# Kernel tuning notes

Hardware: AMD Instinct MI355X
Metric: run time of the kernel (lower is better)

Reference implementation:

```python
import jax, jax.numpy as jnp
import numpy as np

N_NODES = 50000
IN_CH, HID_CH, OUT_CH = 128, 128, 16
N_EDGES = 800000


def setup_inputs() -> dict:
    key = jax.random.key(0)
    ks = jax.random.split(key, 10)
    def lin_w(k, fan_in, fan_out):
        bound = 1.0 / np.sqrt(fan_in)
        return jax.random.uniform(k, (fan_in, fan_out), jnp.float32, -bound, bound)
    inp = {
        'x': jax.random.normal(ks[0], (N_NODES, IN_CH), jnp.float32),
        'edge_index': jax.random.randint(ks[1], (2, N_EDGES), 0, N_NODES, jnp.int64),
        # SAGEConv l/r weights: lin_l (neighbor aggregate, with bias), lin_r (root, no bias)
        'W1_l': lin_w(ks[2], IN_CH, HID_CH), 'b1': jnp.zeros((HID_CH,), jnp.float32),
        'W1_r': lin_w(ks[3], IN_CH, HID_CH),
        'W2_l': lin_w(ks[4], HID_CH, HID_CH), 'b2': jnp.zeros((HID_CH,), jnp.float32),
        'W2_r': lin_w(ks[5], HID_CH, HID_CH),
        'W3_l': lin_w(ks[6], HID_CH, HID_CH), 'b3': jnp.zeros((HID_CH,), jnp.float32),
        'W3_r': lin_w(ks[7], HID_CH, HID_CH),
        'W_lin': lin_w(ks[8], HID_CH, OUT_CH), 'b_lin': jnp.zeros((OUT_CH,), jnp.float32),
    }
    return inp


def _sage_conv(x, src, dst, W_l, b_l, W_r, n_nodes):
    # mean aggregation of source-node features at destination nodes
    msg_sum = jax.ops.segment_sum(x[src], dst, num_segments=n_nodes)  # [N, d]
    deg = jax.ops.segment_sum(jnp.ones((src.shape[0],), x.dtype), dst, num_segments=n_nodes)
    mean = msg_sum / jnp.maximum(deg, 1.0)[:, None]
    return mean @ W_l + b_l + x @ W_r


def reference(x, edge_index, W1_l, b1, W1_r, W2_l, b2, W2_r, W3_l, b3, W3_r, W_lin, b_lin):
    src, dst = edge_index[0], edge_index[1]
    n = x.shape[0]
    h = jax.nn.relu(_sage_conv(x, src, dst, W1_l, b1, W1_r, n))
    h = jax.nn.relu(_sage_conv(h, src, dst, W2_l, b2, W2_r, n))
    # dropout is identity in eval mode
    h = jax.nn.relu(_sage_conv(h, src, dst, W3_l, b3, W3_r, n))
    return h @ W_lin + b_lin
```

## Files before the change

### kernel.cpp

```cpp
#include <hip/hip_runtime.h>


typedef short bf16x8 __attribute__((ext_vector_type(8)));
typedef float f32x4 __attribute__((ext_vector_type(4)));

__device__ __forceinline__ float bf16_to_f32(unsigned int lo16) {
  unsigned int u = lo16 << 16;
  return __builtin_bit_cast(float, u);
}
__device__ __forceinline__ unsigned short f32_to_bf16(float f) {
  unsigned int u = __builtin_bit_cast(unsigned int, f);
  unsigned int r = (u + 0x7FFFu + ((u >> 16) & 1u)) >> 16;
  return (unsigned short)r;
}

__device__ __forceinline__ void gload_lds16(const void* g, void* lds_base) {
  __builtin_amdgcn_global_load_lds(
      (__attribute__((address_space(1))) unsigned int*)(uintptr_t)g,
      (__attribute__((address_space(3))) unsigned int*)(unsigned int)(uintptr_t)lds_base,
      16, 0, 0);
}

__global__ void k_zero_i32(int* __restrict__ p, int n) {
  int i = blockIdx.x * blockDim.x + threadIdx.x;
  if (i < n) p[i] = 0;
}

__global__ __launch_bounds__(256) void k_split(const float* __restrict__ in,
                                               unsigned short* __restrict__ hi,
                                               unsigned short* __restrict__ lo, int n4) {
  int i = blockIdx.x * blockDim.x + threadIdx.x;
  if (i < n4) {
    float4 v = *reinterpret_cast<const float4*>(&in[(size_t)i * 4]);
    ushort4 h, l;
    h.x = f32_to_bf16(v.x); l.x = f32_to_bf16(v.x - bf16_to_f32(h.x));
    h.y = f32_to_bf16(v.y); l.y = f32_to_bf16(v.y - bf16_to_f32(h.y));
    h.z = f32_to_bf16(v.z); l.z = f32_to_bf16(v.z - bf16_to_f32(h.z));
    h.w = f32_to_bf16(v.w); l.w = f32_to_bf16(v.w - bf16_to_f32(h.w));
    *reinterpret_cast<ushort4*>(&hi[(size_t)i * 4]) = h;
    *reinterpret_cast<ushort4*>(&lo[(size_t)i * 4]) = l;
  }
}

__global__ __launch_bounds__(256) void k_prep_w3(
    const float* __restrict__ W1l, const float* __restrict__ W1r,
    const float* __restrict__ W2l, const float* __restrict__ W2r,
    const float* __restrict__ W3l, const float* __restrict__ W3r,
    unsigned short* __restrict__ Whi1, unsigned short* __restrict__ Wlo1,
    unsigned short* __restrict__ Whi2, unsigned short* __restrict__ Wlo2,
    unsigned short* __restrict__ Whi3, unsigned short* __restrict__ Wlo3) {
  int layer = blockIdx.x >> 7;
  int n = blockIdx.x & 127;
  int k = threadIdx.x;
  const float* Wl = (layer == 0) ? W1l : (layer == 1) ? W2l : W3l;
  const float* Wr = (layer == 0) ? W1r : (layer == 1) ? W2r : W3r;
  unsigned short* Whi = (layer == 0) ? Whi1 : (layer == 1) ? Whi2 : Whi3;
  unsigned short* Wlo = (layer == 0) ? Wlo1 : (layer == 1) ? Wlo2 : Wlo3;
  float v = (k < 128) ? Wl[(size_t)k * 128 + n] : Wr[(size_t)(k - 128) * 128 + n];
  unsigned short h = f32_to_bf16(v);
  Whi[(size_t)n * 256 + k] = h;
  Wlo[(size_t)n * 256 + k] = f32_to_bf16(v - bf16_to_f32(h));
}

__global__ void k_detect(const int* __restrict__ ei, int* __restrict__ flag) {
  int t = threadIdx.x;
  if (t == 0) *flag = 0;
  __syncthreads();
  int any = 0;
  for (int i = t; i < 1024; i += 256)
    if (ei[2 * i + 1] != 0) any = 1;
  if (any) atomicOr(flag, 1);
}

__device__ __forceinline__ int load_src(const int* ei, int E, int i, int is32) {
  return is32 ? ei[i] : ei[2 * i];
}
__device__ __forceinline__ int load_dst(const int* ei, int E, int i, int is32) {
  return is32 ? ei[E + i] : ei[2 * E + 2 * i];
}

__global__ __launch_bounds__(256) void k_count(const int* __restrict__ ei,
                                               const int* __restrict__ flag,
                                               int* __restrict__ deg,
                                               int* __restrict__ erank, int E) {
  int i = blockIdx.x * blockDim.x + threadIdx.x;
  if (i < E) {
    int is32 = *flag;
    erank[i] = atomicAdd(&deg[load_dst(ei, E, i, is32)], 1);
  }
}

__global__ __launch_bounds__(256) void k_scan1(const int* __restrict__ deg,
                                               int* __restrict__ bsum, int N) {
  __shared__ int s[256];
  int t = threadIdx.x;
  int base = blockIdx.x * 1024 + t * 4;
  int v = 0;
#pragma unroll
  for (int j = 0; j < 4; ++j) {
    int i = base + j;
    v += (i < N) ? deg[i] : 0;
  }
  s[t] = v;
  __syncthreads();
  for (int off = 128; off > 0; off >>= 1) {
    if (t < off) s[t] += s[t + off];
    __syncthreads();
  }
  if (t == 0) bsum[blockIdx.x] = s[0];
}

__global__ __launch_bounds__(1024) void k_scan2(int* __restrict__ bsum,
                                                int* __restrict__ row_ptr,
                                                int nb, int N) {
  __shared__ int s[1024];
  int t = threadIdx.x;
  int v = (t < nb) ? bsum[t] : 0;
  s[t] = v;
  __syncthreads();
  for (int off = 1; off < 1024; off <<= 1) {
    int add = (t >= off) ? s[t - off] : 0;
    __syncthreads();
    s[t] += add;
    __syncthreads();
  }
  if (t < nb) bsum[t] = s[t] - v;
  if (t == 1023) row_ptr[N] = s[1023];
}

__global__ __launch_bounds__(256) void k_scan3(const int* __restrict__ deg,
                                               const int* __restrict__ bsum,
                                               int* __restrict__ row_ptr,
                                               float* __restrict__ inv_deg, int N) {
  __shared__ int s[256];
  int t = threadIdx.x;
  int base = blockIdx.x * 1024 + t * 4;
  int v[4];
  int sum = 0;
#pragma unroll
  for (int j = 0; j < 4; ++j) {
    int i = base + j;
    v[j] = (i < N) ? deg[i] : 0;
    sum += v[j];
  }
  s[t] = sum;
  __syncthreads();
  for (int off = 1; off < 256; off <<= 1) {
    int add = (t >= off) ? s[t - off] : 0;
    __syncthreads();
    s[t] += add;
    __syncthreads();
  }
  int excl = s[t] - sum + bsum[blockIdx.x];
#pragma unroll
  for (int j = 0; j < 4; ++j) {
    int i = base + j;
    if (i < N) {
      row_ptr[i] = excl;
      inv_deg[i] = 1.0f / (float)((v[j] > 1) ? v[j] : 1);
      excl += v[j];
    }
  }
}

__global__ __launch_bounds__(256) void k_fill(const int* __restrict__ ei,
                                              const int* __restrict__ flag,
                                              const int* __restrict__ row_ptr,
                                              const int* __restrict__ erank,
                                              int* __restrict__ col_idx, int E) {
  int i = blockIdx.x * blockDim.x + threadIdx.x;
  if (i < E) {
    int is32 = *flag;
    int d = load_dst(ei, E, i, is32);
    int s = load_src(ei, E, i, is32);
    col_idx[row_ptr[d] + erank[i]] = s;
  }
}

__global__ __launch_bounds__(256) void k_aggregate(const unsigned short* __restrict__ Xhi,
                                                   const int* __restrict__ row_ptr,
                                                   const int* __restrict__ col_idx,
                                                   const float* __restrict__ inv_deg,
                                                   unsigned int* __restrict__ Mhi,
                                                   unsigned int* __restrict__ Mlo, int N) {
  int gw = (int)((blockIdx.x * blockDim.x + threadIdx.x) >> 6);
  int lane = threadIdx.x & 63;
  if (gw >= N) return;
  int s = row_ptr[gw], e = row_ptr[gw + 1];
  const unsigned int* Xp =
      reinterpret_cast<const unsigned int*>(Xhi) + lane;
  float ax[8], ay[8];
#pragma unroll
  for (int q = 0; q < 8; ++q) { ax[q] = 0.f; ay[q] = 0.f; }
  int j = s;
  for (; j + 8 <= e; j += 8) {
    unsigned int v[8];
#pragma unroll
    for (int q = 0; q < 8; ++q) v[q] = Xp[(size_t)col_idx[j + q] * 64];
#pragma unroll
    for (int q = 0; q < 8; ++q) {
      ax[q] += bf16_to_f32(v[q] & 0xFFFFu);
      ay[q] += bf16_to_f32(v[q] >> 16);
    }
  }
  for (; j + 4 <= e; j += 4) {
    unsigned int v[4];
#pragma unroll
    for (int q = 0; q < 4; ++q) v[q] = Xp[(size_t)col_idx[j + q] * 64];
#pragma unroll
    for (int q = 0; q < 4; ++q) {
      ax[q] += bf16_to_f32(v[q] & 0xFFFFu);
      ay[q] += bf16_to_f32(v[q] >> 16);
    }
  }
  for (; j < e; ++j) {
    unsigned int v = Xp[(size_t)col_idx[j] * 64];
    ax[0] += bf16_to_f32(v & 0xFFFFu);
    ay[0] += bf16_to_f32(v >> 16);
  }
  float inv = inv_deg[gw];
  float rx = ((ax[0] + ax[1]) + (ax[2] + ax[3])) + ((ax[4] + ax[5]) + (ax[6] + ax[7]));
  float ry = ((ay[0] + ay[1]) + (ay[2] + ay[3])) + ((ay[4] + ay[5]) + (ay[6] + ay[7]));
  rx *= inv;
  ry *= inv;
  unsigned int hx = f32_to_bf16(rx), hy = f32_to_bf16(ry);
  unsigned int lx = f32_to_bf16(rx - bf16_to_f32(hx));
  unsigned int ly = f32_to_bf16(ry - bf16_to_f32(hy));
  Mhi[(size_t)gw * 64 + lane] = hx | (hy << 16);
  Mlo[(size_t)gw * 64 + lane] = lx | (ly << 16);
}

__global__ __launch_bounds__(256) void k_mfma_gemm(
    const unsigned short* __restrict__ A1hi, const unsigned short* __restrict__ A1lo,
    const unsigned short* __restrict__ A2hi, const unsigned short* __restrict__ A2lo,
    const unsigned short* __restrict__ Whi, const unsigned short* __restrict__ Wlo,
    const float* __restrict__ bias,
    unsigned short* __restrict__ Ohi, unsigned short* __restrict__ Olo, int N) {
  __shared__ unsigned short sAhi[2][128 * 32], sAlo[2][128 * 32];
  __shared__ unsigned short sBhi[2][128 * 32], sBlo[2][128 * 32];
  int t = threadIdx.x;
  int lane = t & 63;
  int w = t >> 6;
  int wr = (w >> 1) * 64, wc = (w & 1) * 64;
  int block_row = blockIdx.x * 128;

  f32x4 acc[4][4];
#pragma unroll
  for (int m = 0; m < 4; ++m)
#pragma unroll
    for (int n = 0; n < 4; ++n) acc[m][n] = f32x4{0.f, 0.f, 0.f, 0.f};

  int kg = lane & 3;
  int rr = lane >> 2;
  int fr = lane & 15;
  int fkb = (lane >> 4) * 16;

  auto stage = [&](int kt, int b) {
    const unsigned short* gsrc;
    unsigned short* lbase;
    int isA = (w < 2);
    if (w == 0) { gsrc = (kt < 4) ? A1hi : A2hi; lbase = sAhi[b]; }
    else if (w == 1) { gsrc = (kt < 4) ? A1lo : A2lo; lbase = sAlo[b]; }
    else if (w == 2) { gsrc = Whi; lbase = sBhi[b]; }
    else { gsrc = Wlo; lbase = sBlo[b]; }
#pragma unroll
    for (int c = 0; c < 8; ++c) {
      int idx = c * 16 + rr;
      const char* src;
      if (isA) {
        int rg = block_row + idx;
        if (rg > N - 1) rg = N - 1;
        src = (const char*)gsrc + (size_t)rg * 256 + (kt & 3) * 64 + kg * 16;
      } else {
        src = (const char*)gsrc + (size_t)idx * 512 + kt * 64 + kg * 16;
      }
      gload_lds16(src, (char*)lbase + c * 1024);
    }
  };

  stage(0, 0);
  __syncthreads();

  for (int kt = 0; kt < 8; ++kt) {
    int cur = kt & 1;
    if (kt < 7) stage(kt + 1, cur ^ 1);
    bf16x8 a_hi[4], a_lo[4], b_hi[4], b_lo[4];
#pragma unroll
    for (int m = 0; m < 4; ++m) {
      int row = wr + m * 16 + fr;
      a_hi[m] = *reinterpret_cast<const bf16x8*>((const char*)sAhi[cur] + row * 64 + fkb);
      a_lo[m] = *reinterpret_cast<const bf16x8*>((const char*)sAlo[cur] + row * 64 + fkb);
    }
#pragma unroll
    for (int n = 0; n < 4; ++n) {
      int col = wc + n * 16 + fr;
      b_hi[n] = *reinterpret_cast<const bf16x8*>((const char*)sBhi[cur] + col * 64 + fkb);
      b_lo[n] = *reinterpret_cast<const bf16x8*>((const char*)sBlo[cur] + col * 64 + fkb);
    }
#pragma unroll
    for (int m = 0; m < 4; ++m)
#pragma unroll
      for (int n = 0; n < 4; ++n) {
        acc[m][n] = __builtin_amdgcn_mfma_f32_16x16x32_bf16(a_hi[m], b_hi[n], acc[m][n], 0, 0, 0);
        acc[m][n] = __builtin_amdgcn_mfma_f32_16x16x32_bf16(a_hi[m], b_lo[n], acc[m][n], 0, 0, 0);
        acc[m][n] = __builtin_amdgcn_mfma_f32_16x16x32_bf16(a_lo[m], b_hi[n], acc[m][n], 0, 0, 0);
      }
    __syncthreads();
  }

  float bv[4];
#pragma unroll
  for (int n = 0; n < 4; ++n) bv[n] = bias[wc + n * 16 + (lane & 15)];
#pragma unroll
  for (int m = 0; m < 4; ++m) {
#pragma unroll
    for (int n = 0; n < 4; ++n) {
#pragma unroll
      for (int j = 0; j < 4; ++j) {
        int row_l = wr + m * 16 + (lane >> 4) * 4 + j;
        int g = block_row + row_l;
        if (g < N) {
          int col = wc + n * 16 + (lane & 15);
          float v = fmaxf(acc[m][n][j] + bv[n], 0.f);
          unsigned short h = f32_to_bf16(v);
          Ohi[(size_t)g * 128 + col] = h;
          Olo[(size_t)g * 128 + col] = f32_to_bf16(v - bf16_to_f32(h));
        }
      }
    }
  }
}

__global__ __launch_bounds__(256) void k_mfma_gemm_final(
    const unsigned short* __restrict__ A1hi, const unsigned short* __restrict__ A1lo,
    const unsigned short* __restrict__ A2hi, const unsigned short* __restrict__ A2lo,
    const unsigned short* __restrict__ Whi, const unsigned short* __restrict__ Wlo,
    const float* __restrict__ bias,
    const float* __restrict__ Wlin, const float* __restrict__ blin,
    float* __restrict__ Out, int N) {
  __shared__ unsigned short smem[32768];
  int t = threadIdx.x;
  int lane = t & 63;
  int w = t >> 6;
  int wr = (w >> 1) * 64, wc = (w & 1) * 64;
  int block_row = blockIdx.x * 128;

  int kg = lane & 3;
  int rr = lane >> 2;
  int fr = lane & 15;
  int fkb = (lane >> 4) * 16;
  int ke = (lane >> 4) * 8;
  int colw = lane & 15;

  bf16x8 wbh[4], wbl[4];
#pragma unroll
  for (int ks = 0; ks < 4; ++ks) {
#pragma unroll
    for (int e = 0; e < 8; ++e) {
      float wv = Wlin[(size_t)(ks * 32 + ke + e) * 16 + colw];
      unsigned short h = f32_to_bf16(wv);
      wbh[ks][e] = (short)h;
      wbl[ks][e] = (short)f32_to_bf16(wv - bf16_to_f32(h));
    }
  }

  f32x4 acc[4][4];
#pragma unroll
  for (int m = 0; m < 4; ++m)
#pragma unroll
    for (int n = 0; n < 4; ++n) acc[m][n] = f32x4{0.f, 0.f, 0.f, 0.f};

  auto sAhi = [&](int b) { return smem + b * 4096; };
  auto sAlo = [&](int b) { return smem + 8192 + b * 4096; };
  auto sBhi = [&](int b) { return smem + 16384 + b * 4096; };
  auto sBlo = [&](int b) { return smem + 24576 + b * 4096; };

  auto stage = [&](int kt, int b) {
    const unsigned short* gsrc;
    unsigned short* lbase;
    int isA = (w < 2);
    if (w == 0) { gsrc = (kt < 4) ? A1hi : A2hi; lbase = sAhi(b); }
    else if (w == 1) { gsrc = (kt < 4) ? A1lo : A2lo; lbase = sAlo(b); }
    else if (w == 2) { gsrc = Whi; lbase = sBhi(b); }
    else { gsrc = Wlo; lbase = sBlo(b); }
#pragma unroll
    for (int c = 0; c < 8; ++c) {
      int idx = c * 16 + rr;
      const char* src;
      if (isA) {
        int rg = block_row + idx;
        if (rg > N - 1) rg = N - 1;
        src = (const char*)gsrc + (size_t)rg * 256 + (kt & 3) * 64 + kg * 16;
      } else {
        src = (const char*)gsrc + (size_t)idx * 512 + kt * 64 + kg * 16;
      }
      gload_lds16(src, (char*)lbase + c * 1024);
    }
  };

  stage(0, 0);
  __syncthreads();

  for (int kt = 0; kt < 8; ++kt) {
    int cur = kt & 1;
    if (kt < 7) stage(kt + 1, cur ^ 1);
    bf16x8 a_hi[4], a_lo[4], b_hi[4], b_lo[4];
#pragma unroll
    for (int m = 0; m < 4; ++m) {
      int row = wr + m * 16 + fr;
      a_hi[m] = *reinterpret_cast<const bf16x8*>((const char*)sAhi(cur) + row * 64 + fkb);
      a_lo[m] = *reinterpret_cast<const bf16x8*>((const char*)sAlo(cur) + row * 64 + fkb);
    }
#pragma unroll
    for (int n = 0; n < 4; ++n) {
      int col = wc + n * 16 + fr;
      b_hi[n] = *reinterpret_cast<const bf16x8*>((const char*)sBhi(cur) + col * 64 + fkb);
      b_lo[n] = *reinterpret_cast<const bf16x8*>((const char*)sBlo(cur) + col * 64 + fkb);
    }
#pragma unroll
    for (int m = 0; m < 4; ++m)
#pragma unroll
      for (int n = 0; n < 4; ++n) {
        acc[m][n] = __builtin_amdgcn_mfma_f32_16x16x32_bf16(a_hi[m], b_hi[n], acc[m][n], 0, 0, 0);
        acc[m][n] = __builtin_amdgcn_mfma_f32_16x16x32_bf16(a_hi[m], b_lo[n], acc[m][n], 0, 0, 0);
        acc[m][n] = __builtin_amdgcn_mfma_f32_16x16x32_bf16(a_lo[m], b_hi[n], acc[m][n], 0, 0, 0);
      }
    __syncthreads();
  }

  unsigned short* hhi = smem;
  unsigned short* hlo = smem + 16384;
  float bv[4];
#pragma unroll
  for (int n = 0; n < 4; ++n) bv[n] = bias[wc + n * 16 + (lane & 15)];
#pragma unroll
  for (int m = 0; m < 4; ++m) {
#pragma unroll
    for (int n = 0; n < 4; ++n) {
#pragma unroll
      for (int j = 0; j < 4; ++j) {
        int row_l = wr + m * 16 + (lane >> 4) * 4 + j;
        int col = wc + n * 16 + (lane & 15);
        float v = fmaxf(acc[m][n][j] + bv[n], 0.f);
        unsigned short h = f32_to_bf16(v);
        hhi[row_l * 128 + col] = h;
        hlo[row_l * 128 + col] = f32_to_bf16(v - bf16_to_f32(h));
      }
    }
  }
  __syncthreads();

  float bo = blin[colw];
#pragma unroll
  for (int m2 = 0; m2 < 2; ++m2) {
    int mtile = w * 2 + m2;
    f32x4 a2 = f32x4{0.f, 0.f, 0.f, 0.f};
#pragma unroll
    for (int ks = 0; ks < 4; ++ks) {
      int row = mtile * 16 + fr;
      bf16x8 ah = *reinterpret_cast<const bf16x8*>(hhi + row * 128 + ks * 32 + ke);
      bf16x8 al = *reinterpret_cast<const bf16x8*>(hlo + row * 128 + ks * 32 + ke);
      a2 = __builtin_amdgcn_mfma_f32_16x16x32_bf16(ah, wbh[ks], a2, 0, 0, 0);
      a2 = __builtin_amdgcn_mfma_f32_16x16x32_bf16(ah, wbl[ks], a2, 0, 0, 0);
      a2 = __builtin_amdgcn_mfma_f32_16x16x32_bf16(al, wbh[ks], a2, 0, 0, 0);
    }
#pragma unroll
    for (int j = 0; j < 4; ++j) {
      int row = mtile * 16 + (lane >> 4) * 4 + j;
      int g = block_row + row;
      if (g < N) Out[(size_t)g * 16 + colw] = a2[j] + bo;
    }
  }
}

extern "C" void kernel_launch(void* const* d_in, const int* in_sizes, int n_in,
                              void* d_out, int out_size, void* d_ws, size_t ws_size,
                              hipStream_t stream) {
  if (n_in < 13) return;
  const float* x = (const float*)d_in[0];
  const int* ei = (const int*)d_in[1];
  const float* W1l = (const float*)d_in[2];
  const float* b1 = (const float*)d_in[3];
  const float* W1r = (const float*)d_in[4];
  const float* W2l = (const float*)d_in[5];
  const float* b2 = (const float*)d_in[6];
  const float* W2r = (const float*)d_in[7];
  const float* W3l = (const float*)d_in[8];
  const float* b3 = (const float*)d_in[9];
  const float* W3r = (const float*)d_in[10];
  const float* Wlin = (const float*)d_in[11];
  const float* blin = (const float*)d_in[12];
  float* out = (float*)d_out;

  const int N = in_sizes[0] / 128;
  const int E = in_sizes[1] / 2;

  char* w = (char*)d_ws;
  size_t off = 0;
  auto alloc = [&](size_t bytes) -> void* {
    off = (off + 255) & ~(size_t)255;
    void* p = (void*)(w + off);
    off += bytes;
    return p;
  };
  size_t actB = (size_t)N * 128 * 2;
  unsigned short* Xhi = (unsigned short*)alloc(actB);
  unsigned short* Xlo = (unsigned short*)alloc(actB);
  unsigned short* Ahi = (unsigned short*)alloc(actB);
  unsigned short* Alo = (unsigned short*)alloc(actB);
  unsigned short* Mhi = (unsigned short*)alloc(actB);
  unsigned short* Mlo = (unsigned short*)alloc(actB);
  unsigned short* Wt[6];
  for (int i = 0; i < 6; ++i) Wt[i] = (unsigned short*)alloc(128 * 256 * 2);
  int* deg = (int*)alloc((size_t)N * 4);
  int* row_ptr = (int*)alloc((size_t)(N + 1) * 4);
  int* col_idx = (int*)alloc((size_t)E * 4);
  int* erank = (int*)alloc((size_t)E * 4);
  float* invdeg = (float*)alloc((size_t)N * 4);
  int* flag = (int*)alloc(4);
  int* bsum = (int*)alloc((size_t)1024 * 4);
  (void)ws_size;

  const int nbScan = (N + 1023) / 1024;

  k_zero_i32<<<(N + 255) / 256, 256, 0, stream>>>(deg, N);
  k_detect<<<1, 256, 0, stream>>>(ei, flag);
  k_count<<<(E + 255) / 256, 256, 0, stream>>>(ei, flag, deg, erank, E);
  k_split<<<(N * 32 + 255) / 256, 256, 0, stream>>>(x, Xhi, Xlo, N * 32);
  k_prep_w3<<<384, 256, 0, stream>>>(W1l, W1r, W2l, W2r, W3l, W3r,
                                     Wt[0], Wt[1], Wt[2], Wt[3], Wt[4], Wt[5]);
  k_scan1<<<nbScan, 256, 0, stream>>>(deg, bsum, N);
  k_scan2<<<1, 1024, 0, stream>>>(bsum, row_ptr, nbScan, N);
  k_scan3<<<nbScan, 256, 0, stream>>>(deg, bsum, row_ptr, invdeg, N);
  k_fill<<<(E + 255) / 256, 256, 0, stream>>>(ei, flag, row_ptr, erank, col_idx, E);

  int aggBlocks = (N * 64 + 255) / 256;
  int gemmBlocks = (N + 127) / 128;

  k_aggregate<<<aggBlocks, 256, 0, stream>>>(Xhi, row_ptr, col_idx, invdeg,
                                             (unsigned int*)Mhi, (unsigned int*)Mlo, N);
  k_mfma_gemm<<<gemmBlocks, 256, 0, stream>>>(Mhi, Mlo, Xhi, Xlo, Wt[0], Wt[1], b1,
                                              Ahi, Alo, N);
  k_aggregate<<<aggBlocks, 256, 0, stream>>>(Ahi, row_ptr, col_idx, invdeg,
                                             (unsigned int*)Mhi, (unsigned int*)Mlo, N);
  k_mfma_gemm<<<gemmBlocks, 256, 0, stream>>>(Mhi, Mlo, Ahi, Alo, Wt[2], Wt[3], b2,
                                              Xhi, Xlo, N);
  k_aggregate<<<aggBlocks, 256, 0, stream>>>(Xhi, row_ptr, col_idx, invdeg,
                                             (unsigned int*)Mhi, (unsigned int*)Mlo, N);
  k_mfma_gemm_final<<<gemmBlocks, 256, 0, stream>>>(Mhi, Mlo, Xhi, Xlo, Wt[4], Wt[5],
                                                    b3, Wlin, blin, out, N);
}
```

Measured before the change: 245.2 us.

## Load weight fragments directly from global memory and stage only activations in LDS

Both MFMA GEMM kernels stop staging the weight (B) tiles through LDS. Each wave now reads its weight fragments straight from global memory, which the small, heavily shared weight matrix should serve from cache. All four waves now split the activation (A) staging, and the K loop is fully unrolled. This halves the shared-memory footprint and the async-copy work per tile, which may raise occupancy, but it adds direct global loads, now exposed in latency, inside the MFMA loop.

```diff
diff --git a/kernel.cpp b/kernel.cpp
--- a/kernel.cpp
+++ b/kernel.cpp
@@ -236,8 +236,7 @@
     const unsigned short* __restrict__ Whi, const unsigned short* __restrict__ Wlo,
     const float* __restrict__ bias,
     unsigned short* __restrict__ Ohi, unsigned short* __restrict__ Olo, int N) {
-  __shared__ unsigned short sAhi[2][128 * 32], sAlo[2][128 * 32];
-  __shared__ unsigned short sBhi[2][128 * 32], sBlo[2][128 * 32];
+  __shared__ unsigned short sAhi[2][4096], sAlo[2][4096];
   int t = threadIdx.x;
   int lane = t & 63;
   int w = t >> 6;
@@ -254,48 +253,44 @@
   int rr = lane >> 2;
   int fr = lane & 15;
   int fkb = (lane >> 4) * 16;
-
-  auto stage = [&](int kt, int b) {
-    const unsigned short* gsrc;
-    unsigned short* lbase;
-    int isA = (w < 2);
-    if (w == 0) { gsrc = (kt < 4) ? A1hi : A2hi; lbase = sAhi[b]; }
-    else if (w == 1) { gsrc = (kt < 4) ? A1lo : A2lo; lbase = sAlo[b]; }
-    else if (w == 2) { gsrc = Whi; lbase = sBhi[b]; }
-    else { gsrc = Wlo; lbase = sBlo[b]; }
-#pragma unroll
-    for (int c = 0; c < 8; ++c) {
+  int half = w >> 1;
+  int quarter = w & 1;
+
+  auto stageA = [&](int kt, int b) {
+    const unsigned short* gsrc = (half == 0) ? ((kt < 4) ? A1hi : A2hi)
+                                             : ((kt < 4) ? A1lo : A2lo);
+    unsigned short* lbase = (half == 0) ? &sAhi[b][0] : &sAlo[b][0];
+#pragma unroll
+    for (int cc = 0; cc < 4; ++cc) {
+      int c = quarter * 4 + cc;
       int idx = c * 16 + rr;
-      const char* src;
-      if (isA) {
-        int rg = block_row + idx;
-        if (rg > N - 1) rg = N - 1;
-        src = (const char*)gsrc + (size_t)rg * 256 + (kt & 3) * 64 + kg * 16;
-      } else {
-        src = (const char*)gsrc + (size_t)idx * 512 + kt * 64 + kg * 16;
-      }
+      int rg = block_row + idx;
+      if (rg > N - 1) rg = N - 1;
+      const char* src = (const char*)gsrc + (size_t)rg * 256 + (kt & 3) * 64 + kg * 16;
       gload_lds16(src, (char*)lbase + c * 1024);
     }
   };
 
-  stage(0, 0);
-  __syncthreads();
-
+  stageA(0, 0);
+  __syncthreads();
+
+#pragma unroll
   for (int kt = 0; kt < 8; ++kt) {
     int cur = kt & 1;
-    if (kt < 7) stage(kt + 1, cur ^ 1);
-    bf16x8 a_hi[4], a_lo[4], b_hi[4], b_lo[4];
+    if (kt < 7) stageA(kt + 1, cur ^ 1);
+    bf16x8 b_hi[4], b_lo[4];
+#pragma unroll
+    for (int n = 0; n < 4; ++n) {
+      int col = wc + n * 16 + fr;
+      b_hi[n] = *reinterpret_cast<const bf16x8*>((const char*)Whi + (size_t)col * 512 + kt * 64 + fkb);
+      b_lo[n] = *reinterpret_cast<const bf16x8*>((const char*)Wlo + (size_t)col * 512 + kt * 64 + fkb);
+    }
+    bf16x8 a_hi[4], a_lo[4];
 #pragma unroll
     for (int m = 0; m < 4; ++m) {
       int row = wr + m * 16 + fr;
-      a_hi[m] = *reinterpret_cast<const bf16x8*>((const char*)sAhi[cur] + row * 64 + fkb);
-      a_lo[m] = *reinterpret_cast<const bf16x8*>((const char*)sAlo[cur] + row * 64 + fkb);
-    }
-#pragma unroll
-    for (int n = 0; n < 4; ++n) {
-      int col = wc + n * 16 + fr;
-      b_hi[n] = *reinterpret_cast<const bf16x8*>((const char*)sBhi[cur] + col * 64 + fkb);
-      b_lo[n] = *reinterpret_cast<const bf16x8*>((const char*)sBlo[cur] + col * 64 + fkb);
+      a_hi[m] = *reinterpret_cast<const bf16x8*>((const char*)&sAhi[cur][0] + row * 64 + fkb);
+      a_lo[m] = *reinterpret_cast<const bf16x8*>((const char*)&sAlo[cur][0] + row * 64 + fkb);
     }
 #pragma unroll
     for (int m = 0; m < 4; ++m)
@@ -351,6 +346,8 @@
   int fkb = (lane >> 4) * 16;
   int ke = (lane >> 4) * 8;
   int colw = lane & 15;
+  int half = w >> 1;
+  int quarter = w & 1;
 
   bf16x8 wbh[4], wbl[4];
 #pragma unroll
@@ -372,50 +369,42 @@
 
   auto sAhi = [&](int b) { return smem + b * 4096; };
   auto sAlo = [&](int b) { return smem + 8192 + b * 4096; };
-  auto sBhi = [&](int b) { return smem + 16384 + b * 4096; };
-  auto sBlo = [&](int b) { return smem + 24576 + b * 4096; };
-
-  auto stage = [&](int kt, int b) {
-    const unsigned short* gsrc;
-    unsigned short* lbase;
-    int isA = (w < 2);
-    if (w == 0) { gsrc = (kt < 4) ? A1hi : A2hi; lbase = sAhi(b); }
-    else if (w == 1) { gsrc = (kt < 4) ? A1lo : A2lo; lbase = sAlo(b); }
-    else if (w == 2) { gsrc = Whi; lbase = sBhi(b); }
-    else { gsrc = Wlo; lbase = sBlo(b); }
-#pragma unroll
-    for (int c = 0; c < 8; ++c) {
+
+  auto stageA = [&](int kt, int b) {
+    const unsigned short* gsrc = (half == 0) ? ((kt < 4) ? A1hi : A2hi)
+                                             : ((kt < 4) ? A1lo : A2lo);
+    unsigned short* lbase = (half == 0) ? sAhi(b) : sAlo(b);
+#pragma unroll
+    for (int cc = 0; cc < 4; ++cc) {
+      int c = quarter * 4 + cc;
       int idx = c * 16 + rr;
-      const char* src;
-      if (isA) {
-        int rg = block_row + idx;
-        if (rg > N - 1) rg = N - 1;
-        src = (const char*)gsrc + (size_t)rg * 256 + (kt & 3) * 64 + kg * 16;
-      } else {
-        src = (const char*)gsrc + (size_t)idx * 512 + kt * 64 + kg * 16;
-      }
+      int rg = block_row + idx;
+      if (rg > N - 1) rg = N - 1;
+      const char* src = (const char*)gsrc + (size_t)rg * 256 + (kt & 3) * 64 + kg * 16;
       gload_lds16(src, (char*)lbase + c * 1024);
     }
   };
 
-  stage(0, 0);
-  __syncthreads();
-
+  stageA(0, 0);
+  __syncthreads();
+
+#pragma unroll
   for (int kt = 0; kt < 8; ++kt) {
     int cur = kt & 1;
-    if (kt < 7) stage(kt + 1, cur ^ 1);
-    bf16x8 a_hi[4], a_lo[4], b_hi[4], b_lo[4];
+    if (kt < 7) stageA(kt + 1, cur ^ 1);
+    bf16x8 b_hi[4], b_lo[4];
+#pragma unroll
+    for (int n = 0; n < 4; ++n) {
+      int col = wc + n * 16 + fr;
+      b_hi[n] = *reinterpret_cast<const bf16x8*>((const char*)Whi + (size_t)col * 512 + kt * 64 + fkb);
+      b_lo[n] = *reinterpret_cast<const bf16x8*>((const char*)Wlo + (size_t)col * 512 + kt * 64 + fkb);
+    }
+    bf16x8 a_hi[4], a_lo[4];
 #pragma unroll
     for (int m = 0; m < 4; ++m) {
       int row = wr + m * 16 + fr;
       a_hi[m] = *reinterpret_cast<const bf16x8*>((const char*)sAhi(cur) + row * 64 + fkb);
       a_lo[m] = *reinterpret_cast<const bf16x8*>((const char*)sAlo(cur) + row * 64 + fkb);
-    }
-#pragma unroll
-    for (int n = 0; n < 4; ++n) {
-      int col = wc + n * 16 + fr;
-      b_hi[n] = *reinterpret_cast<const bf16x8*>((const char*)sBhi(cur) + col * 64 + fkb);
-      b_lo[n] = *reinterpret_cast<const bf16x8*>((const char*)sBlo(cur) + col * 64 + fkb);
     }
 #pragma unroll
     for (int m = 0; m < 4; ++m)
```

Measured after the change: 285.2 us. 16.3% more time.
